# Kernel tuning notes

Hardware: AMD Instinct MI355X
Metric: run time of the kernel (lower is better)

## Reference

```python
import jax, jax.numpy as jnp
import numpy as np

IN_C, C_M, C_N, K = 512, 512, 128, 1
B, H, W = 8, 64, 64

def setup_inputs() -> dict:
    key = jax.random.key(0)
    ks = jax.random.split(key, 8)
    s = 1.0 / np.sqrt(IN_C)
    return {
        "x": jax.random.normal(ks[0], (B, IN_C, H, W), dtype=jnp.float32),
        "y": jax.random.normal(ks[1], (B, C_M, H, W), dtype=jnp.float32),
        "wA": jax.random.uniform(ks[2], (C_M, IN_C), minval=-s, maxval=s, dtype=jnp.float32),
        "bA": jax.random.uniform(ks[3], (C_M,), minval=-s, maxval=s, dtype=jnp.float32),
        "wB": jax.random.uniform(ks[4], (C_N, IN_C), minval=-s, maxval=s, dtype=jnp.float32),
        "bB": jax.random.uniform(ks[5], (C_N,), minval=-s, maxval=s, dtype=jnp.float32),
        "wV": jax.random.uniform(ks[6], (C_N, IN_C), minval=-s, maxval=s, dtype=jnp.float32),
        "bV": jax.random.uniform(ks[7], (C_N,), minval=-s, maxval=s, dtype=jnp.float32),
    }

def reference(x, y, wA, bA, wB, bB, wV, bV):
    # A2-Net double attention, K=1 so batch = b1 and K*h*w = N.
    b, c, h, w = x.shape
    N = h * w
    xf = x.reshape(b, c, N)                                  # [b, C, N]
    A = jnp.einsum('mc,bcn->bmn', wA, xf) + bA[:, None]      # [b, c_m, N]
    Bf = jnp.einsum('kc,bcn->bkn', wB, xf) + bB[:, None]     # [b, c_n, N]
    V = jnp.einsum('kc,bcn->bkn', wV, xf) + bV[:, None]      # [b, c_n, N]
    # tmpB viewed (b*c_n, N), softmax dim=1 -> softmax over N per (b, c_n) row
    softB = jax.nn.softmax(Bf, axis=-1)                      # [b, c_n, N]
    # tmpV viewed (b*N, c_n), softmax dim=1 -> softmax over c_n per pixel
    softV = jax.nn.softmax(V, axis=1)                        # [b, c_n, N]
    # gather: tmpG = tmpA @ softB^T  -> [b, c_m, c_n]
    G = jnp.einsum('bmn,bkn->bmk', A, softB)
    # distribute: tmpZ = G @ softV -> [b, c_m, N]
    Z = jnp.einsum('bmk,bkn->bmn', G, softV)
    return Z.reshape(b, -1, h, w) + y
```

## Files before the change

### kernel.cpp

```cpp
#include <hip/hip_runtime.h>

#define BATCH 8
#define INC 512
#define CM 512
#define CN 128
#define NPIX 4096
#define NSPLIT 16

typedef short bf16x8 __attribute__((ext_vector_type(8)));
typedef float f32x4 __attribute__((ext_vector_type(4)));
typedef unsigned short us8v __attribute__((ext_vector_type(8)));

__device__ __forceinline__ unsigned short f2b(float f) {
    union { float f; unsigned u; } v; v.f = f;
    unsigned r = v.u + 0x7FFF + ((v.u >> 16) & 1);
    return (unsigned short)(r >> 16);
}
__device__ __forceinline__ float b2f(unsigned short u) {
    union { unsigned u; float f; } v; v.u = ((unsigned)u) << 16;
    return v.f;
}

__device__ __forceinline__ void gl_lds16(const unsigned short* g, unsigned short* l) {
    __builtin_amdgcn_global_load_lds(
        (const __attribute__((address_space(1))) unsigned int*)g,
        (__attribute__((address_space(3))) unsigned int*)l, 16, 0, 0);
}

__device__ __forceinline__ void stage_tile(const unsigned short* src, int ld, int kbase,
                                           unsigned short* lds, int t) {
    #pragma unroll
    for (int q = 0; q < 2; ++q) {
        int f = q * 256 + t;
        const unsigned short* g = src + (size_t)(f >> 2) * ld + kbase + (f & 3) * 8;
        gl_lds16(g, lds + f * 8);
    }
}

__device__ __forceinline__ void bt_compute(const unsigned short* lA, const unsigned short* lB,
                                           f32x4 acc[4][4], int wr, int wc, int lane) {
    int lr = lane & 15, lq = lane >> 4;
    bf16x8 av[4], bv[4];
    #pragma unroll
    for (int i = 0; i < 4; ++i)
        av[i] = *(const bf16x8*)&lA[(wr * 64 + i * 16 + lr) * 32 + lq * 8];
    #pragma unroll
    for (int j = 0; j < 4; ++j)
        bv[j] = *(const bf16x8*)&lB[(wc * 64 + j * 16 + lr) * 32 + lq * 8];
    #pragma unroll
    for (int i = 0; i < 4; ++i)
        #pragma unroll
        for (int j = 0; j < 4; ++j)
            acc[i][j] = __builtin_amdgcn_mfma_f32_16x16x32_bf16(av[i], bv[j], acc[i][j], 0, 0, 0);
}

#define ZERO_ACC(acc)                       \
    f32x4 acc[4][4];                        \
    {                                       \
        f32x4 z4 = {0.f, 0.f, 0.f, 0.f};   \
        for (int i = 0; i < 4; ++i)         \
            for (int j = 0; j < 4; ++j)     \
                acc[i][j] = z4;             \
    }

__global__ __launch_bounds__(256) void k_prep_w(
    const float* __restrict__ wA, const float* __restrict__ wB, const float* __restrict__ wV,
    unsigned short* __restrict__ wA16, unsigned short* __restrict__ wB16,
    unsigned short* __restrict__ wV16)
{
    int e = (blockIdx.x * 256 + threadIdx.x) * 4;
    const float* src; unsigned short* dst; int off;
    if (e < 262144)       { src = wA; dst = wA16; off = e; }
    else if (e < 327680)  { src = wB; dst = wB16; off = e - 262144; }
    else                  { src = wV; dst = wV16; off = e - 327680; }
    float4 v = *(const float4*)&src[off];
    ushort4 u = make_ushort4(f2b(v.x), f2b(v.y), f2b(v.z), f2b(v.w));
    *(ushort4*)&dst[off] = u;
}

__global__ __launch_bounds__(256) void k_transpose(
    const float* __restrict__ x, unsigned short* __restrict__ xT)
{
    __shared__ unsigned short tile[64][68];
    int n0 = blockIdx.x * 64, c0 = blockIdx.y * 64, b = blockIdx.z;
    int t = threadIdx.x;
    int tr = t >> 4, tc4 = (t & 15) * 4;
    const float* xb = x + ((size_t)b * INC + c0) * NPIX + n0;
    #pragma unroll
    for (int p = 0; p < 4; ++p) {
        int r = p * 16 + tr;
        float4 v = *(const float4*)&xb[(size_t)r * NPIX + tc4];
        tile[r][tc4 + 0] = f2b(v.x); tile[r][tc4 + 1] = f2b(v.y);
        tile[r][tc4 + 2] = f2b(v.z); tile[r][tc4 + 3] = f2b(v.w);
    }
    __syncthreads();
    unsigned short* o = xT + ((size_t)b * NPIX + n0) * INC + c0;
    #pragma unroll
    for (int p = 0; p < 4; ++p) {
        int n = p * 16 + tr;
        ushort4 u = make_ushort4(tile[tc4 + 0][n], tile[tc4 + 1][n],
                                 tile[tc4 + 2][n], tile[tc4 + 3][n]);
        *(ushort4*)&o[(size_t)n * INC + tc4] = u;
    }
}

__global__ __launch_bounds__(256) void k_proj(
    const unsigned short* __restrict__ xT, const unsigned short* __restrict__ wB16,
    const unsigned short* __restrict__ wV16, const float* __restrict__ bB,
    const float* __restrict__ bV, unsigned short* __restrict__ Bf16,
    unsigned short* __restrict__ V16)
{
    __shared__ unsigned short lA[128 * 32], lB[128 * 32];
    int t = threadIdx.x;
    int n0 = blockIdx.x * 128;
    int z = blockIdx.y, b = z >> 1, br = z & 1;
    const unsigned short* A = br ? wV16 : wB16;
    const float* bias = br ? bV : bB;
    unsigned short* out = br ? V16 : Bf16;
    const unsigned short* Bm = xT + ((size_t)b * NPIX + n0) * INC;

    ZERO_ACC(acc);
    int lane = t & 63, w = t >> 6, wr = w >> 1, wc = w & 1;

    for (int c = 0; c < INC; c += 32) {
        stage_tile(A, INC, c, lA, t);
        stage_tile(Bm, INC, c, lB, t);
        __syncthreads();
        bt_compute(lA, lB, acc, wr, wc, lane);
        __syncthreads();
    }
    int lr = lane & 15, lq = lane >> 4;
    #pragma unroll
    for (int i = 0; i < 4; ++i)
        #pragma unroll
        for (int reg = 0; reg < 4; ++reg) {
            int k = wr * 64 + i * 16 + lq * 4 + reg;
            float bv_ = bias[k];
            #pragma unroll
            for (int j = 0; j < 4; ++j) {
                int n = n0 + wc * 64 + j * 16 + lr;
                out[((size_t)b * CN + k) * NPIX + n] = f2b(acc[i][j][reg] + bv_);
            }
        }
}

__global__ __launch_bounds__(256) void k_softmax_rows(
    const unsigned short* __restrict__ Bf16, unsigned short* __restrict__ sB)
{
    __shared__ float red[8];
    int row = blockIdx.x, t = threadIdx.x;
    const unsigned short* p = Bf16 + (size_t)row * NPIX + t * 16;
    us8v u0 = *(const us8v*)p, u1 = *(const us8v*)(p + 8);
    float v[16];
    #pragma unroll
    for (int j = 0; j < 8; ++j) { v[j] = b2f(u0[j]); v[8 + j] = b2f(u1[j]); }
    float m = -1e30f;
    #pragma unroll
    for (int j = 0; j < 16; ++j) m = fmaxf(m, v[j]);
    for (int o = 32; o > 0; o >>= 1) m = fmaxf(m, __shfl_xor(m, o));
    if ((t & 63) == 0) red[t >> 6] = m;
    __syncthreads();
    m = fmaxf(fmaxf(red[0], red[1]), fmaxf(red[2], red[3]));
    float s = 0.f;
    #pragma unroll
    for (int j = 0; j < 16; ++j) { v[j] = __expf(v[j] - m); s += v[j]; }
    for (int o = 32; o > 0; o >>= 1) s += __shfl_xor(s, o);
    if ((t & 63) == 0) red[4 + (t >> 6)] = s;
    __syncthreads();
    float r = 1.0f / (red[4] + red[5] + red[6] + red[7]);
    us8v o0, o1;
    #pragma unroll
    for (int j = 0; j < 8; ++j) { o0[j] = f2b(v[j] * r); o1[j] = f2b(v[8 + j] * r); }
    unsigned short* q = sB + (size_t)row * NPIX + t * 16;
    *(us8v*)q = o0; *(us8v*)(q + 8) = o1;
}

__global__ __launch_bounds__(256) void k_softmax_cols(
    const unsigned short* __restrict__ V16, unsigned short* __restrict__ sVt)
{
    __shared__ unsigned short tv[128][138];
    __shared__ float sm[128], sr[128];
    int n0 = blockIdx.x * 128, b = blockIdx.y, t = threadIdx.x;
    const unsigned short* vb = V16 + (size_t)b * CN * NPIX;
    #pragma unroll 4
    for (int it = 0; it < 64; ++it) {
        int idx = it * 256 + t, k = idx >> 7, nl = idx & 127;
        tv[nl][k] = vb[(size_t)k * NPIX + n0 + nl];
    }
    __syncthreads();
    if (t < 128) {
        float m = -1e30f;
        for (int k = 0; k < 128; ++k) m = fmaxf(m, b2f(tv[t][k]));
        float s = 0.f;
        for (int k = 0; k < 128; ++k) s += __expf(b2f(tv[t][k]) - m);
        sm[t] = m; sr[t] = 1.0f / s;
    }
    __syncthreads();
    unsigned short* ob = sVt + ((size_t)b * NPIX + n0) * CN;
    #pragma unroll
    for (int it = 0; it < 8; ++it) {
        int idx = it * 2048 + t * 8, nl = idx >> 7, k0 = idx & 127;
        float m = sm[nl], r = sr[nl];
        us8v o;
        #pragma unroll
        for (int j = 0; j < 8; ++j) o[j] = f2b(__expf(b2f(tv[nl][k0 + j]) - m) * r);
        *(us8v*)&ob[(size_t)nl * CN + k0] = o;
    }
}

__global__ __launch_bounds__(256) void k_gather(
    const float* __restrict__ x, const unsigned short* __restrict__ sB,
    float* __restrict__ Pts)
{
    __shared__ unsigned short lA[128 * 32], lB[128 * 32];
    int t = threadIdx.x;
    int c0 = blockIdx.x * 128, s = blockIdx.y, b = blockIdx.z;
    const unsigned short* A = sB + (size_t)b * CN * NPIX;
    const float* xb = x + ((size_t)b * INC + c0) * NPIX;
    int nbase = s * (NPIX / NSPLIT);

    ZERO_ACC(acc);
    int lane = t & 63, w = t >> 6, wr = w >> 1, wc = w & 1;

    for (int it = 0; it < (NPIX / NSPLIT) / 32; ++it) {
        int nb = nbase + it * 32;
        stage_tile(A, NPIX, nb, lA, t);
        #pragma unroll
        for (int q = 0; q < 4; ++q) {
            int f = q * 256 + t, r = f >> 3, nof = (f & 7) * 4;
            float4 v = *(const float4*)&xb[(size_t)r * NPIX + nb + nof];
            ushort4 u = make_ushort4(f2b(v.x), f2b(v.y), f2b(v.z), f2b(v.w));
            *(ushort4*)&lB[r * 32 + nof] = u;
        }
        __syncthreads();
        bt_compute(lA, lB, acc, wr, wc, lane);
        __syncthreads();
    }
    int lr = lane & 15, lq = lane >> 4;
    #pragma unroll
    for (int i = 0; i < 4; ++i)
        #pragma unroll
        for (int reg = 0; reg < 4; ++reg) {
            int k = wr * 64 + i * 16 + lq * 4 + reg;
            #pragma unroll
            for (int j = 0; j < 4; ++j) {
                int cc = wc * 64 + j * 16 + lr;
                Pts[(((size_t)s * BATCH + b) * CN + k) * INC + c0 + cc] = acc[i][j][reg];
            }
        }
}

__global__ __launch_bounds__(256) void k_reduceP(
    const float* __restrict__ Pts, unsigned short* __restrict__ Pt16)
{
    int base = (blockIdx.x * 256 + threadIdx.x) * 4;
    float4 sacc = make_float4(0.f, 0.f, 0.f, 0.f);
    #pragma unroll
    for (int sp = 0; sp < NSPLIT; ++sp) {
        float4 v = *(const float4*)&Pts[(size_t)sp * (BATCH * CN * INC) + base];
        sacc.x += v.x; sacc.y += v.y; sacc.z += v.z; sacc.w += v.w;
    }
    *(ushort4*)&Pt16[base] = make_ushort4(f2b(sacc.x), f2b(sacc.y), f2b(sacc.z), f2b(sacc.w));
}

__global__ __launch_bounds__(256) void k_G(
    const unsigned short* __restrict__ wA16, const float* __restrict__ bA,
    const unsigned short* __restrict__ Pt16, unsigned short* __restrict__ G16)
{
    __shared__ unsigned short lA[128 * 32], lB[128 * 32];
    int t = threadIdx.x;
    int m0 = blockIdx.x * 128, b = blockIdx.y;
    const unsigned short* A = wA16 + (size_t)m0 * INC;
    const unsigned short* Bm = Pt16 + (size_t)b * CN * INC;

    ZERO_ACC(acc);
    int lane = t & 63, w = t >> 6, wr = w >> 1, wc = w & 1;

    for (int c = 0; c < INC; c += 32) {
        stage_tile(A, INC, c, lA, t);
        stage_tile(Bm, INC, c, lB, t);
        __syncthreads();
        bt_compute(lA, lB, acc, wr, wc, lane);
        __syncthreads();
    }
    int lr = lane & 15, lq = lane >> 4;
    #pragma unroll
    for (int i = 0; i < 4; ++i)
        #pragma unroll
        for (int reg = 0; reg < 4; ++reg) {
            int m = m0 + wr * 64 + i * 16 + lq * 4 + reg;
            float bv_ = bA[m];
            #pragma unroll
            for (int j = 0; j < 4; ++j) {
                int kc = wc * 64 + j * 16 + lr;
                G16[((size_t)b * CM + m) * CN + kc] = f2b(acc[i][j][reg] + bv_);
            }
        }
}

__global__ __launch_bounds__(256) void k_Z(
    const unsigned short* __restrict__ G16, const unsigned short* __restrict__ sVt,
    const float* __restrict__ y, float* __restrict__ out)
{
    __shared__ unsigned short lA[128 * 32], lB[128 * 32];
    int t = threadIdx.x;
    int n0 = blockIdx.x * 128, m0 = blockIdx.y * 128, b = blockIdx.z;
    const unsigned short* A = G16 + ((size_t)b * CM + m0) * CN;
    const unsigned short* Bm = sVt + ((size_t)b * NPIX + n0) * CN;

    ZERO_ACC(acc);
    int lane = t & 63, w = t >> 6, wr = w >> 1, wc = w & 1;

    for (int kc = 0; kc < CN; kc += 32) {
        stage_tile(A, CN, kc, lA, t);
        stage_tile(Bm, CN, kc, lB, t);
        __syncthreads();
        bt_compute(lA, lB, acc, wr, wc, lane);
        __syncthreads();
    }
    int lr = lane & 15, lq = lane >> 4;
    #pragma unroll
    for (int i = 0; i < 4; ++i)
        #pragma unroll
        for (int reg = 0; reg < 4; ++reg) {
            int m = m0 + wr * 64 + i * 16 + lq * 4 + reg;
            #pragma unroll
            for (int j = 0; j < 4; ++j) {
                int n = n0 + wc * 64 + j * 16 + lr;
                size_t idx = ((size_t)b * CM + m) * NPIX + n;
                out[idx] = acc[i][j][reg] + y[idx];
            }
        }
}

extern "C" void kernel_launch(void* const* d_in, const int* in_sizes, int n_in,
                              void* d_out, int out_size, void* d_ws, size_t ws_size,
                              hipStream_t stream)
{
    const float* x  = (const float*)d_in[0];
    const float* y  = (const float*)d_in[1];
    const float* wA = (const float*)d_in[2];
    const float* bA = (const float*)d_in[3];
    const float* wB = (const float*)d_in[4];
    const float* bB = (const float*)d_in[5];
    const float* wV = (const float*)d_in[6];
    const float* bV = (const float*)d_in[7];
    float* out = (float*)d_out;

    unsigned short* xT16 = (unsigned short*)d_ws;
    unsigned short* wA16 = xT16 + 16777216;
    unsigned short* wB16 = wA16 + 262144;
    unsigned short* wV16 = wB16 + 65536;
    unsigned short* Bf16 = wV16 + 65536;
    unsigned short* V16  = Bf16 + 4194304;
    unsigned short* sB   = V16  + 4194304;
    unsigned short* sVt  = sB   + 4194304;
    unsigned short* Pt16 = sVt  + 4194304;
    float*  Pts = (float*)(Pt16 + 524288);
    unsigned short* G16  = (unsigned short*)(Pts + (size_t)NSPLIT * BATCH * CN * INC);

    k_prep_w<<<384, 256, 0, stream>>>(wA, wB, wV, wA16, wB16, wV16);
    k_transpose<<<dim3(NPIX / 64, INC / 64, BATCH), 256, 0, stream>>>(x, xT16);
    k_proj<<<dim3(NPIX / 128, BATCH * 2), 256, 0, stream>>>(xT16, wB16, wV16, bB, bV, Bf16, V16);
    k_softmax_rows<<<dim3(BATCH * CN), 256, 0, stream>>>(Bf16, sB);
    k_softmax_cols<<<dim3(NPIX / 128, BATCH), 256, 0, stream>>>(V16, sVt);
    k_gather<<<dim3(INC / 128, NSPLIT, BATCH), 256, 0, stream>>>(x, sB, Pts);
    k_reduceP<<<512, 256, 0, stream>>>(Pts, Pt16);
    k_G<<<dim3(CM / 128, BATCH), 256, 0, stream>>>(wA16, bA, Pt16, G16);
    k_Z<<<dim3(NPIX / 128, CM / 128, BATCH), 256, 0, stream>>>(G16, sVt, y, out);
}
```

Baseline: 273.0 us.

## Stage GEMM epilogues through LDS, merge prep kernels, precompute bf16 x for gather

Fuses weight conversion and x transpose into one kernel that also writes a non-transposed bf16 copy of x, so the gather GEMM stages bf16 tiles directly instead of converting fp32 x inside every tile load. All GEMM epilogues now go through a padded LDS buffer to produce row-contiguous vectorized global stores in place of scattered scalar stores. The column softmax uses vectorized loads and splits the max/sum over 256 threads, and NSPLIT is halved so there are fewer partial sums to reduce. The costs are an extra 32 MB workspace write for x16, extra barriers in each epilogue, and fewer gather blocks.

New measurement: 265.6 us. 1.03x faster.

```diff
diff --git a/kernel.cpp b/kernel.cpp
--- a/kernel.cpp
+++ b/kernel.cpp
@@ -5,7 +5,7 @@
 #define CM 512
 #define CN 128
 #define NPIX 4096
-#define NSPLIT 16
+#define NSPLIT 8
 
 typedef short bf16x8 __attribute__((ext_vector_type(8)));
 typedef float f32x4 __attribute__((ext_vector_type(4)));
@@ -63,35 +63,56 @@
                 acc[i][j] = z4;             \
     }
 
-__global__ __launch_bounds__(256) void k_prep_w(
-    const float* __restrict__ wA, const float* __restrict__ wB, const float* __restrict__ wV,
+__device__ __forceinline__ void ep_stage(float* ep, const f32x4 (*acc)[4],
+                                         int ch, int wr, int wc, int lane) {
+    if (wr == (ch >> 1)) {
+        int lr = lane & 15, lq = lane >> 4;
+        int ibase = (ch & 1) * 2;
+        #pragma unroll
+        for (int ii = 0; ii < 2; ++ii) {
+            #pragma unroll
+            for (int j = 0; j < 4; ++j)
+                #pragma unroll
+                for (int reg = 0; reg < 4; ++reg)
+                    ep[(ii * 16 + lq * 4 + reg) * 132 + wc * 64 + j * 16 + lr] =
+                        acc[ibase + ii][j][reg];
+        }
+    }
+}
+
+__global__ __launch_bounds__(256) void k_prep(
+    const float* __restrict__ x, const float* __restrict__ wA,
+    const float* __restrict__ wB, const float* __restrict__ wV,
+    unsigned short* __restrict__ xT, unsigned short* __restrict__ x16,
     unsigned short* __restrict__ wA16, unsigned short* __restrict__ wB16,
     unsigned short* __restrict__ wV16)
 {
-    int e = (blockIdx.x * 256 + threadIdx.x) * 4;
-    const float* src; unsigned short* dst; int off;
-    if (e < 262144)       { src = wA; dst = wA16; off = e; }
-    else if (e < 327680)  { src = wB; dst = wB16; off = e - 262144; }
-    else                  { src = wV; dst = wV16; off = e - 327680; }
-    float4 v = *(const float4*)&src[off];
-    ushort4 u = make_ushort4(f2b(v.x), f2b(v.y), f2b(v.z), f2b(v.w));
-    *(ushort4*)&dst[off] = u;
-}
-
-__global__ __launch_bounds__(256) void k_transpose(
-    const float* __restrict__ x, unsigned short* __restrict__ xT)
-{
+    if (blockIdx.z == BATCH) {
+        int bl = blockIdx.y * 64 + blockIdx.x;
+        if (bl >= 384) return;
+        int e = (bl * 256 + threadIdx.x) * 4;
+        const float* src; unsigned short* dst; int off;
+        if (e < 262144)       { src = wA; dst = wA16; off = e; }
+        else if (e < 327680)  { src = wB; dst = wB16; off = e - 262144; }
+        else                  { src = wV; dst = wV16; off = e - 327680; }
+        float4 v = *(const float4*)&src[off];
+        *(ushort4*)&dst[off] = make_ushort4(f2b(v.x), f2b(v.y), f2b(v.z), f2b(v.w));
+        return;
+    }
     __shared__ unsigned short tile[64][68];
     int n0 = blockIdx.x * 64, c0 = blockIdx.y * 64, b = blockIdx.z;
     int t = threadIdx.x;
     int tr = t >> 4, tc4 = (t & 15) * 4;
     const float* xb = x + ((size_t)b * INC + c0) * NPIX + n0;
+    unsigned short* x16p = x16 + ((size_t)b * INC + c0) * NPIX + n0;
     #pragma unroll
     for (int p = 0; p < 4; ++p) {
         int r = p * 16 + tr;
         float4 v = *(const float4*)&xb[(size_t)r * NPIX + tc4];
-        tile[r][tc4 + 0] = f2b(v.x); tile[r][tc4 + 1] = f2b(v.y);
-        tile[r][tc4 + 2] = f2b(v.z); tile[r][tc4 + 3] = f2b(v.w);
+        ushort4 u = make_ushort4(f2b(v.x), f2b(v.y), f2b(v.z), f2b(v.w));
+        *(ushort4*)&x16p[(size_t)r * NPIX + tc4] = u;
+        tile[r][tc4 + 0] = u.x; tile[r][tc4 + 1] = u.y;
+        tile[r][tc4 + 2] = u.z; tile[r][tc4 + 3] = u.w;
     }
     __syncthreads();
     unsigned short* o = xT + ((size_t)b * NPIX + n0) * INC + c0;
@@ -110,7 +131,9 @@
     const float* __restrict__ bV, unsigned short* __restrict__ Bf16,
     unsigned short* __restrict__ V16)
 {
-    __shared__ unsigned short lA[128 * 32], lB[128 * 32];
+    __shared__ __align__(16) char smem[32 * 132 * 4];
+    unsigned short* lA = (unsigned short*)smem;
+    unsigned short* lB = lA + 4096;
     int t = threadIdx.x;
     int n0 = blockIdx.x * 128;
     int z = blockIdx.y, b = z >> 1, br = z & 1;
@@ -129,19 +152,24 @@
         bt_compute(lA, lB, acc, wr, wc, lane);
         __syncthreads();
     }
-    int lr = lane & 15, lq = lane >> 4;
-    #pragma unroll
-    for (int i = 0; i < 4; ++i)
-        #pragma unroll
-        for (int reg = 0; reg < 4; ++reg) {
-            int k = wr * 64 + i * 16 + lq * 4 + reg;
-            float bv_ = bias[k];
+    float* ep = (float*)smem;
+    #pragma unroll
+    for (int ch = 0; ch < 4; ++ch) {
+        __syncthreads();
+        ep_stage(ep, acc, ch, wr, wc, lane);
+        __syncthreads();
+        int r = t >> 3, c4 = (t & 7) * 16;
+        int k = ch * 32 + r;
+        float bv_ = bias[k];
+        unsigned short* op = out + ((size_t)b * CN + k) * NPIX + n0 + c4;
+        #pragma unroll
+        for (int h = 0; h < 2; ++h) {
+            us8v o;
             #pragma unroll
-            for (int j = 0; j < 4; ++j) {
-                int n = n0 + wc * 64 + j * 16 + lr;
-                out[((size_t)b * CN + k) * NPIX + n] = f2b(acc[i][j][reg] + bv_);
-            }
+            for (int j = 0; j < 8; ++j) o[j] = f2b(ep[r * 132 + c4 + h * 8 + j] + bv_);
+            *(us8v*)&op[h * 8] = o;
         }
+    }
 }
 
 __global__ __launch_bounds__(256) void k_softmax_rows(
@@ -179,20 +207,30 @@
     const unsigned short* __restrict__ V16, unsigned short* __restrict__ sVt)
 {
     __shared__ unsigned short tv[128][138];
-    __shared__ float sm[128], sr[128];
+    __shared__ float pm[2][128], ps[2][128], sm[128], sr[128];
     int n0 = blockIdx.x * 128, b = blockIdx.y, t = threadIdx.x;
-    const unsigned short* vb = V16 + (size_t)b * CN * NPIX;
-    #pragma unroll 4
-    for (int it = 0; it < 64; ++it) {
-        int idx = it * 256 + t, k = idx >> 7, nl = idx & 127;
-        tv[nl][k] = vb[(size_t)k * NPIX + n0 + nl];
+    const unsigned short* vb = V16 + (size_t)b * CN * NPIX + n0;
+    #pragma unroll
+    for (int it = 0; it < 8; ++it) {
+        int f = it * 256 + t, k = f >> 4, n8 = (f & 15) * 8;
+        us8v u = *(const us8v*)&vb[(size_t)k * NPIX + n8];
+        #pragma unroll
+        for (int j = 0; j < 8; ++j) tv[n8 + j][k] = u[j];
+    }
+    __syncthreads();
+    {
+        int p = t & 127, h = t >> 7;
+        float m = -1e30f;
+        for (int k = h * 64; k < h * 64 + 64; ++k) m = fmaxf(m, b2f(tv[p][k]));
+        float s = 0.f;
+        for (int k = h * 64; k < h * 64 + 64; ++k) s += __expf(b2f(tv[p][k]) - m);
+        pm[h][p] = m; ps[h][p] = s;
     }
     __syncthreads();
     if (t < 128) {
-        float m = -1e30f;
-        for (int k = 0; k < 128; ++k) m = fmaxf(m, b2f(tv[t][k]));
-        float s = 0.f;
-        for (int k = 0; k < 128; ++k) s += __expf(b2f(tv[t][k]) - m);
+        float ma = pm[0][t], mb = pm[1][t];
+        float m = fmaxf(ma, mb);
+        float s = ps[0][t] * __expf(ma - m) + ps[1][t] * __expf(mb - m);
         sm[t] = m; sr[t] = 1.0f / s;
     }
     __syncthreads();
@@ -209,14 +247,16 @@
 }
 
 __global__ __launch_bounds__(256) void k_gather(
-    const float* __restrict__ x, const unsigned short* __restrict__ sB,
+    const unsigned short* __restrict__ x16, const unsigned short* __restrict__ sB,
     float* __restrict__ Pts)
 {
-    __shared__ unsigned short lA[128 * 32], lB[128 * 32];
+    __shared__ __align__(16) char smem[32 * 132 * 4];
+    unsigned short* lA = (unsigned short*)smem;
+    unsigned short* lB = lA + 4096;
     int t = threadIdx.x;
     int c0 = blockIdx.x * 128, s = blockIdx.y, b = blockIdx.z;
     const unsigned short* A = sB + (size_t)b * CN * NPIX;
-    const float* xb = x + ((size_t)b * INC + c0) * NPIX;
+    const unsigned short* Bm = x16 + ((size_t)b * INC + c0) * NPIX;
     int nbase = s * (NPIX / NSPLIT);
 
     ZERO_ACC(acc);
@@ -225,29 +265,24 @@
     for (int it = 0; it < (NPIX / NSPLIT) / 32; ++it) {
         int nb = nbase + it * 32;
         stage_tile(A, NPIX, nb, lA, t);
-        #pragma unroll
-        for (int q = 0; q < 4; ++q) {
-            int f = q * 256 + t, r = f >> 3, nof = (f & 7) * 4;
-            float4 v = *(const float4*)&xb[(size_t)r * NPIX + nb + nof];
-            ushort4 u = make_ushort4(f2b(v.x), f2b(v.y), f2b(v.z), f2b(v.w));
-            *(ushort4*)&lB[r * 32 + nof] = u;
-        }
+        stage_tile(Bm, NPIX, nb, lB, t);
         __syncthreads();
         bt_compute(lA, lB, acc, wr, wc, lane);
         __syncthreads();
     }
-    int lr = lane & 15, lq = lane >> 4;
-    #pragma unroll
-    for (int i = 0; i < 4; ++i)
-        #pragma unroll
-        for (int reg = 0; reg < 4; ++reg) {
-            int k = wr * 64 + i * 16 + lq * 4 + reg;
-            #pragma unroll
-            for (int j = 0; j < 4; ++j) {
-                int cc = wc * 64 + j * 16 + lr;
-                Pts[(((size_t)s * BATCH + b) * CN + k) * INC + c0 + cc] = acc[i][j][reg];
-            }
-        }
+    float* ep = (float*)smem;
+    #pragma unroll
+    for (int ch = 0; ch < 4; ++ch) {
+        __syncthreads();
+        ep_stage(ep, acc, ch, wr, wc, lane);
+        __syncthreads();
+        int r = t >> 3, c4 = (t & 7) * 16;
+        int k = ch * 32 + r;
+        float* op = &Pts[(((size_t)s * BATCH + b) * CN + k) * INC + c0 + c4];
+        #pragma unroll
+        for (int q = 0; q < 4; ++q)
+            *(float4*)&op[q * 4] = *(float4*)&ep[r * 132 + c4 + q * 4];
+    }
 }
 
 __global__ __launch_bounds__(256) void k_reduceP(
@@ -267,7 +302,9 @@
     const unsigned short* __restrict__ wA16, const float* __restrict__ bA,
     const unsigned short* __restrict__ Pt16, unsigned short* __restrict__ G16)
 {
-    __shared__ unsigned short lA[128 * 32], lB[128 * 32];
+    __shared__ __align__(16) char smem[32 * 132 * 4];
+    unsigned short* lA = (unsigned short*)smem;
+    unsigned short* lB = lA + 4096;
     int t = threadIdx.x;
     int m0 = blockIdx.x * 128, b = blockIdx.y;
     const unsigned short* A = wA16 + (size_t)m0 * INC;
@@ -283,26 +320,33 @@
         bt_compute(lA, lB, acc, wr, wc, lane);
         __syncthreads();
     }
-    int lr = lane & 15, lq = lane >> 4;
-    #pragma unroll
-    for (int i = 0; i < 4; ++i)
-        #pragma unroll
-        for (int reg = 0; reg < 4; ++reg) {
-            int m = m0 + wr * 64 + i * 16 + lq * 4 + reg;
-            float bv_ = bA[m];
+    float* ep = (float*)smem;
+    #pragma unroll
+    for (int ch = 0; ch < 4; ++ch) {
+        __syncthreads();
+        ep_stage(ep, acc, ch, wr, wc, lane);
+        __syncthreads();
+        int r = t >> 3, c4 = (t & 7) * 16;
+        int m = m0 + ch * 32 + r;
+        float bv_ = bA[m];
+        unsigned short* op = G16 + ((size_t)b * CM + m) * CN + c4;
+        #pragma unroll
+        for (int h = 0; h < 2; ++h) {
+            us8v o;
             #pragma unroll
-            for (int j = 0; j < 4; ++j) {
-                int kc = wc * 64 + j * 16 + lr;
-                G16[((size_t)b * CM + m) * CN + kc] = f2b(acc[i][j][reg] + bv_);
-            }
+            for (int j = 0; j < 8; ++j) o[j] = f2b(ep[r * 132 + c4 + h * 8 + j] + bv_);
+            *(us8v*)&op[h * 8] = o;
         }
+    }
 }
 
 __global__ __launch_bounds__(256) void k_Z(
     const unsigned short* __restrict__ G16, const unsigned short* __restrict__ sVt,
     const float* __restrict__ y, float* __restrict__ out)
 {
-    __shared__ unsigned short lA[128 * 32], lB[128 * 32];
+    __shared__ __align__(16) char smem[32 * 132 * 4];
+    unsigned short* lA = (unsigned short*)smem;
+    unsigned short* lB = lA + 4096;
     int t = threadIdx.x;
     int n0 = blockIdx.x * 128, m0 = blockIdx.y * 128, b = blockIdx.z;
     const unsigned short* A = G16 + ((size_t)b * CM + m0) * CN;
@@ -318,19 +362,23 @@
         bt_compute(lA, lB, acc, wr, wc, lane);
         __syncthreads();
     }
-    int lr = lane & 15, lq = lane >> 4;
-    #pragma unroll
-    for (int i = 0; i < 4; ++i)
-        #pragma unroll
-        for (int reg = 0; reg < 4; ++reg) {
-            int m = m0 + wr * 64 + i * 16 + lq * 4 + reg;
-            #pragma unroll
-            for (int j = 0; j < 4; ++j) {
-                int n = n0 + wc * 64 + j * 16 + lr;
-                size_t idx = ((size_t)b * CM + m) * NPIX + n;
-                out[idx] = acc[i][j][reg] + y[idx];
-            }
+    float* ep = (float*)smem;
+    #pragma unroll
+    for (int ch = 0; ch < 4; ++ch) {
+        __syncthreads();
+        ep_stage(ep, acc, ch, wr, wc, lane);
+        __syncthreads();
+        int r = t >> 3, c4 = (t & 7) * 16;
+        int m = m0 + ch * 32 + r;
+        size_t base = ((size_t)b * CM + m) * NPIX + n0 + c4;
+        #pragma unroll
+        for (int q = 0; q < 4; ++q) {
+            float4 a = *(float4*)&ep[r * 132 + c4 + q * 4];
+            float4 yv = *(const float4*)&y[base + q * 4];
+            a.x += yv.x; a.y += yv.y; a.z += yv.z; a.w += yv.w;
+            *(float4*)&out[base + q * 4] = a;
         }
+    }
 }
 
 extern "C" void kernel_launch(void* const* d_in, const int* in_sizes, int n_in,
@@ -348,7 +396,8 @@
     float* out = (float*)d_out;
 
     unsigned short* xT16 = (unsigned short*)d_ws;
-    unsigned short* wA16 = xT16 + 16777216;
+    unsigned short* x16  = xT16 + 16777216;
+    unsigned short* wA16 = x16  + 16777216;
     unsigned short* wB16 = wA16 + 262144;
     unsigned short* wV16 = wB16 + 65536;
     unsigned short* Bf16 = wV16 + 65536;
@@ -359,12 +408,13 @@
     float*  Pts = (float*)(Pt16 + 524288);
     unsigned short* G16  = (unsigned short*)(Pts + (size_t)NSPLIT * BATCH * CN * INC);
 
-    k_prep_w<<<384, 256, 0, stream>>>(wA, wB, wV, wA16, wB16, wV16);
-    k_transpose<<<dim3(NPIX / 64, INC / 64, BATCH), 256, 0, stream>>>(x, xT16);
-    k_proj<<<dim3(NPIX / 128, BATCH * 2), 256, 0, stream>>>(xT16, wB16, wV16, bB, bV, Bf16, V16);
+    k_prep<<<dim3(64, 8, BATCH + 1), 256, 0, stream>>>(
+        x, wA, wB, wV, xT16, x16, wA16, wB16, wV16);
+    k_proj<<<dim3(NPIX / 128, BATCH * 2), 256, 0, stream>>>(
+        xT16, wB16, wV16, bB, bV, Bf16, V16);
     k_softmax_rows<<<dim3(BATCH * CN), 256, 0, stream>>>(Bf16, sB);
     k_softmax_cols<<<dim3(NPIX / 128, BATCH), 256, 0, stream>>>(V16, sVt);
-    k_gather<<<dim3(INC / 128, NSPLIT, BATCH), 256, 0, stream>>>(x, sB, Pts);
+    k_gather<<<dim3(INC / 128, NSPLIT, BATCH), 256, 0, stream>>>(x16, sB, Pts);
     k_reduceP<<<512, 256, 0, stream>>>(Pts, Pt16);
     k_G<<<dim3(CM / 128, BATCH), 256, 0, stream>>>(wA16, bA, Pt16, G16);
     k_Z<<<dim3(NPIX / 128, CM / 128, BATCH), 256, 0, stream>>>(G16, sVt, y, out);
```
